# Optimization experiments

Hardware: AMD Instinct MI355X
Metric: run time of the kernel (lower is better)

Reference implementation:

```python
import jax, jax.numpy as jnp
import numpy as np

H = 64      # hidden_size
L = 4       # num_layers
IN = 28     # input_size
OUT = 10    # output classes


def setup_inputs() -> dict:
    key = jax.random.key(0)
    ks = jax.random.split(key, 2 + 4 * L + 2)
    B, T = 4096, 256
    inp = {"x": jax.random.normal(ks[0], (B, T, IN), jnp.float32)}
    s = 1.0 / np.sqrt(H).astype(np.float32)  # PyTorch LSTM init range
    k = 1
    for l in range(L):
        d_in = IN if l == 0 else H
        inp[f"W_ih{l}"] = jax.random.uniform(ks[k], (4 * H, d_in), jnp.float32, -s, s); k += 1
        inp[f"W_hh{l}"] = jax.random.uniform(ks[k], (4 * H, H), jnp.float32, -s, s); k += 1
        inp[f"b_ih{l}"] = jax.random.uniform(ks[k], (4 * H,), jnp.float32, -s, s); k += 1
        inp[f"b_hh{l}"] = jax.random.uniform(ks[k], (4 * H,), jnp.float32, -s, s); k += 1
    so = 1.0 / np.sqrt(H).astype(np.float32)
    inp["W_out"] = jax.random.uniform(ks[k], (OUT, H), jnp.float32, -so, so); k += 1
    inp["b_out"] = jax.random.uniform(ks[k], (OUT,), jnp.float32, -so, so)
    return inp


def _lstm_layer(x, W_ih, W_hh, b_ih, b_hh):
    # x: [B, T, D] -> h sequence [B, T, H]. PyTorch gate order: i, f, g, o.
    B = x.shape[0]
    gx = jnp.einsum('btd,gd->btg', x, W_ih) + (b_ih + b_hh)  # precompute input gates [B,T,4H]

    def step(carry, gxt):
        h, c = carry
        g = gxt + h @ W_hh.T                      # [B, 4H]
        i = jax.nn.sigmoid(g[:, 0*H:1*H])
        f = jax.nn.sigmoid(g[:, 1*H:2*H])
        gg = jnp.tanh(g[:, 2*H:3*H])
        o = jax.nn.sigmoid(g[:, 3*H:4*H])
        c = f * c + i * gg
        h = o * jnp.tanh(c)
        return (h, c), h

    init = (jnp.zeros((B, H), x.dtype), jnp.zeros((B, H), x.dtype))
    _, hs = jax.lax.scan(step, init, gx.swapaxes(0, 1))  # [T, B, H]
    return hs.swapaxes(0, 1)


def reference(x, W_ih0, W_hh0, b_ih0, b_hh0, W_ih1, W_hh1, b_ih1, b_hh1,
              W_ih2, W_hh2, b_ih2, b_hh2, W_ih3, W_hh3, b_ih3, b_hh3,
              W_out, b_out):
    params = [(W_ih0, W_hh0, b_ih0, b_hh0), (W_ih1, W_hh1, b_ih1, b_hh1),
              (W_ih2, W_hh2, b_ih2, b_hh2), (W_ih3, W_hh3, b_ih3, b_hh3)]
    h = x
    for (W_ih, W_hh, b_ih, b_hh) in params:
        h = _lstm_layer(h, W_ih, W_hh, b_ih, b_hh)
    # final linear on last timestep: r_out[:, -1, :] @ W_out.T + b_out
    return h[:, -1, :] @ W_out.T + b_out
```

## Files before the change

### kernel.cpp

```cpp
#include <hip/hip_runtime.h>

#define TS    256
#define ROWS  16
#define DIN   28

typedef _Float16 f16x4 __attribute__((ext_vector_type(4)));
typedef float    f32x4 __attribute__((ext_vector_type(4)));

#if __has_builtin(__builtin_amdgcn_rcpf)
#define RCPF(x) __builtin_amdgcn_rcpf(x)
#else
#define RCPF(x) (1.0f / (x))
#endif
#if __has_builtin(__builtin_amdgcn_exp2f)
#define EXP2F(x) __builtin_amdgcn_exp2f(x)
#else
#define EXP2F(x) exp2f(x)
#endif

__device__ __forceinline__ float sigm(float x) {
  return RCPF(1.0f + EXP2F(x * -1.44269504f));
}
__device__ __forceinline__ float tanhf_(float x) {
  return 1.0f - 2.0f * RCPF(1.0f + EXP2F(x * 2.885390082f));
}
__device__ __forceinline__ f16x4 cvt4(float a, float b, float c, float d) {
  f16x4 r; r[0] = (_Float16)a; r[1] = (_Float16)b; r[2] = (_Float16)c; r[3] = (_Float16)d;
  return r;
}
__device__ __forceinline__ f16x4 cvt4v(float4 v) { return cvt4(v.x, v.y, v.z, v.w); }

#define MFMA16(a, b, c) __builtin_amdgcn_mfma_f32_16x16x16f16((a), (b), (c), 0, 0, 0)

__global__ __launch_bounds__(1024, 4) void lstm4_pipe(
    const float* __restrict__ x,
    const float* __restrict__ Wih0, const float* __restrict__ Whh0,
    const float* __restrict__ bih0, const float* __restrict__ bhh0,
    const float* __restrict__ Wih1, const float* __restrict__ Whh1,
    const float* __restrict__ bih1, const float* __restrict__ bhh1,
    const float* __restrict__ Wih2, const float* __restrict__ Whh2,
    const float* __restrict__ bih2, const float* __restrict__ bhh2,
    const float* __restrict__ Wih3, const float* __restrict__ Whh3,
    const float* __restrict__ bih3, const float* __restrict__ bhh3,
    const float* __restrict__ Wout, const float* __restrict__ bout,
    float* __restrict__ out)
{
  const int tid  = (int)threadIdx.x;
  const int lane = tid & 63;
  const int w    = tid >> 6;
  const int l    = w >> 2;
  const int wv   = w & 3;
  const int r    = lane & 15;
  const int q    = lane >> 4;
  const int r0   = (int)blockIdx.x * ROWS;

  __shared__ _Float16 hbuf[4][2][ROWS][72];

  for (int i = tid; i < 4 * 2 * ROWS * 72; i += 1024)
    (&hbuf[0][0][0][0])[i] = (_Float16)0.0f;

  const float* Wih = (l == 0) ? Wih0 : (l == 1) ? Wih1 : (l == 2) ? Wih2 : Wih3;
  const float* Whh = (l == 0) ? Whh0 : (l == 1) ? Whh1 : (l == 2) ? Whh2 : Whh3;
  const float* bih = (l == 0) ? bih0 : (l == 1) ? bih1 : (l == 2) ? bih2 : bih3;
  const float* bhh = (l == 0) ? bhh0 : (l == 1) ? bhh1 : (l == 2) ? bhh2 : bhh3;

  f16x4 wx[4][4];
  f16x4 wh[4][4];
  float bv[4];

#pragma unroll
  for (int nt = 0; nt < 4; ++nt) {
    const int col = 64 * nt + 16 * wv + r;
    if (l == 0) {
      wx[nt][0] = cvt4v(*(const float4*)&Wih[col * DIN + 4 * q]);
      wx[nt][1] = (q < 3) ? cvt4v(*(const float4*)&Wih[col * DIN + 16 + 4 * q])
                          : cvt4(0.f, 0.f, 0.f, 0.f);
      wx[nt][2] = cvt4(0.f, 0.f, 0.f, 0.f);
      wx[nt][3] = cvt4(0.f, 0.f, 0.f, 0.f);
    } else {
#pragma unroll
      for (int s = 0; s < 4; ++s)
        wx[nt][s] = cvt4v(*(const float4*)&Wih[col * 64 + 16 * s + 4 * q]);
    }
#pragma unroll
    for (int s = 0; s < 4; ++s)
      wh[nt][s] = cvt4v(*(const float4*)&Whh[col * 64 + 16 * s + 4 * q]);
    bv[nt] = bih[col] + bhh[col];
  }

  const float* xrow = x + (size_t)(r0 + r) * (TS * DIN);
  f16x4 xa0 = cvt4(0.f, 0.f, 0.f, 0.f), xa1 = cvt4(0.f, 0.f, 0.f, 0.f);
  if (l == 0) {
    xa0 = cvt4v(*(const float4*)&xrow[4 * q]);
    if (q < 3) xa1 = cvt4v(*(const float4*)&xrow[16 + 4 * q]);
  }

  f32x4 cst = f32x4{0.f, 0.f, 0.f, 0.f};

  for (int s = 0; s < TS + 3; ++s) {
    __syncthreads();
    const int t = s - l;
    if (t < 0 || t >= TS) continue;
    const int pi = t & 1;

    f32x4 acc[4];
#pragma unroll
    for (int nt = 0; nt < 4; ++nt)
      acc[nt] = f32x4{bv[nt], bv[nt], bv[nt], bv[nt]};

    if (l == 0) {
#pragma unroll
      for (int nt = 0; nt < 4; ++nt) acc[nt] = MFMA16(xa0, wx[nt][0], acc[nt]);
#pragma unroll
      for (int nt = 0; nt < 4; ++nt) acc[nt] = MFMA16(xa1, wx[nt][1], acc[nt]);
      if (t + 1 < TS) {
        const float4 v0 = *(const float4*)&xrow[(t + 1) * DIN + 4 * q];
        float4 v1 = make_float4(0.f, 0.f, 0.f, 0.f);
        if (q < 3) v1 = *(const float4*)&xrow[(t + 1) * DIN + 16 + 4 * q];
        xa0 = cvt4v(v0);
        xa1 = cvt4v(v1);
      }
    } else {
      const _Float16* pin = &hbuf[l - 1][pi][r][4 * q];
#pragma unroll
      for (int s2 = 0; s2 < 4; ++s2) {
        const f16x4 a = *(const f16x4*)&pin[16 * s2];
#pragma unroll
        for (int nt = 0; nt < 4; ++nt) acc[nt] = MFMA16(a, wx[nt][s2], acc[nt]);
      }
    }
    {
      const _Float16* prc = &hbuf[l][pi ^ 1][r][4 * q];
#pragma unroll
      for (int s2 = 0; s2 < 4; ++s2) {
        const f16x4 a = *(const f16x4*)&prc[16 * s2];
#pragma unroll
        for (int nt = 0; nt < 4; ++nt) acc[nt] = MFMA16(a, wh[nt][s2], acc[nt]);
      }
    }

    _Float16* pw = &hbuf[l][pi][4 * q][16 * wv + r];
#pragma unroll
    for (int j = 0; j < 4; ++j) {
      const float ig = sigm(acc[0][j]);
      const float fg = sigm(acc[1][j]);
      const float gg = tanhf_(acc[2][j]);
      const float og = sigm(acc[3][j]);
      const float c  = fg * cst[j] + ig * gg;
      cst[j] = c;
      pw[j * 72] = (_Float16)(og * tanhf_(c));
    }
  }

  __syncthreads();

  if (tid < 160) {
    const int rr = tid & 15;
    const int oc = tid >> 4;
    float a = bout[oc];
#pragma unroll 16
    for (int k = 0; k < 64; ++k)
      a += (float)hbuf[3][1][rr][k] * Wout[oc * 64 + k];
    out[(size_t)(r0 + rr) * 10 + oc] = a;
  }
}

extern "C" void kernel_launch(void* const* d_in, const int* in_sizes, int n_in,
                              void* d_out, int out_size, void* d_ws, size_t ws_size,
                              hipStream_t stream) {
  (void)in_sizes; (void)n_in; (void)d_ws; (void)ws_size; (void)out_size;
  lstm4_pipe<<<dim3(4096 / ROWS), dim3(1024), 0, stream>>>(
      (const float*)d_in[0],
      (const float*)d_in[1],  (const float*)d_in[2],  (const float*)d_in[3],  (const float*)d_in[4],
      (const float*)d_in[5],  (const float*)d_in[6],  (const float*)d_in[7],  (const float*)d_in[8],
      (const float*)d_in[9],  (const float*)d_in[10], (const float*)d_in[11], (const float*)d_in[12],
      (const float*)d_in[13], (const float*)d_in[14], (const float*)d_in[15], (const float*)d_in[16],
      (const float*)d_in[17], (const float*)d_in[18],
      (float*)d_out);
}
```

Before: 505.6 us.

## Replace per-step block barriers with LDS flag sync and use 16x16x32 MFMA

Drops the block-wide __syncthreads per wavefront step. Each layer's waves now wait on per-wave shared-memory progress flags, written with release stores and read by spin-waits, and the h buffer grows to a 4-slot ring so layers can drift up to a few timesteps apart. It also switches to the 16x16x32 f16 MFMA, halving the number of matrix instructions, and moves the next-x global load ahead of the wait. The risks are spin-wait polling overhead and subtle memory-ordering correctness with the volatile flag reads.

```diff
diff --git a/kernel.cpp b/kernel.cpp
--- a/kernel.cpp
+++ b/kernel.cpp
@@ -4,7 +4,7 @@
 #define ROWS  16
 #define DIN   28
 
-typedef _Float16 f16x4 __attribute__((ext_vector_type(4)));
+typedef _Float16 f16x8 __attribute__((ext_vector_type(8)));
 typedef float    f32x4 __attribute__((ext_vector_type(4)));
 
 #if __has_builtin(__builtin_amdgcn_rcpf)
@@ -24,15 +24,26 @@
 __device__ __forceinline__ float tanhf_(float x) {
   return 1.0f - 2.0f * RCPF(1.0f + EXP2F(x * 2.885390082f));
 }
-__device__ __forceinline__ f16x4 cvt4(float a, float b, float c, float d) {
-  f16x4 r; r[0] = (_Float16)a; r[1] = (_Float16)b; r[2] = (_Float16)c; r[3] = (_Float16)d;
+__device__ __forceinline__ f16x8 cvt8(float4 a, float4 b) {
+  f16x8 r;
+  r[0] = (_Float16)a.x; r[1] = (_Float16)a.y; r[2] = (_Float16)a.z; r[3] = (_Float16)a.w;
+  r[4] = (_Float16)b.x; r[5] = (_Float16)b.y; r[6] = (_Float16)b.z; r[7] = (_Float16)b.w;
   return r;
 }
-__device__ __forceinline__ f16x4 cvt4v(float4 v) { return cvt4(v.x, v.y, v.z, v.w); }
-
-#define MFMA16(a, b, c) __builtin_amdgcn_mfma_f32_16x16x16f16((a), (b), (c), 0, 0, 0)
-
-__global__ __launch_bounds__(1024, 4) void lstm4_pipe(
+
+#define MFMA32(a, b, c) __builtin_amdgcn_mfma_f32_16x16x32_f16((a), (b), (c), 0, 0, 0)
+
+__device__ __forceinline__ int imin(int a, int b) { return a < b ? a : b; }
+
+__device__ __forceinline__ void wait4(volatile int* f, int T) {
+  int a = f[0], b = f[1], c = f[2], d = f[3];
+  while (imin(imin(a, b), imin(c, d)) < T) {
+    __builtin_amdgcn_s_sleep(1);
+    a = f[0]; b = f[1]; c = f[2]; d = f[3];
+  }
+}
+
+__global__ __launch_bounds__(1024, 4) void lstm4_flags(
     const float* __restrict__ x,
     const float* __restrict__ Wih0, const float* __restrict__ Whh0,
     const float* __restrict__ bih0, const float* __restrict__ bhh0,
@@ -54,92 +65,101 @@
   const int q    = lane >> 4;
   const int r0   = (int)blockIdx.x * ROWS;
 
-  __shared__ _Float16 hbuf[4][2][ROWS][72];
-
-  for (int i = tid; i < 4 * 2 * ROWS * 72; i += 1024)
+  __shared__ _Float16 hbuf[4][4][ROWS][72] __attribute__((aligned(16)));
+  __shared__ int flags[4][4][4] __attribute__((aligned(16)));
+
+  for (int i = tid; i < 4 * 4 * ROWS * 72; i += 1024)
     (&hbuf[0][0][0][0])[i] = (_Float16)0.0f;
+  if (tid < 64) (&flags[0][0][0])[tid] = -1;
+  __syncthreads();
 
   const float* Wih = (l == 0) ? Wih0 : (l == 1) ? Wih1 : (l == 2) ? Wih2 : Wih3;
   const float* Whh = (l == 0) ? Whh0 : (l == 1) ? Whh1 : (l == 2) ? Whh2 : Whh3;
   const float* bih = (l == 0) ? bih0 : (l == 1) ? bih1 : (l == 2) ? bih2 : bih3;
   const float* bhh = (l == 0) ? bhh0 : (l == 1) ? bhh1 : (l == 2) ? bhh2 : bhh3;
 
-  f16x4 wx[4][4];
-  f16x4 wh[4][4];
+  f16x8 wx[4][2];
+  f16x8 wh[4][2];
   float bv[4];
 
 #pragma unroll
   for (int nt = 0; nt < 4; ++nt) {
     const int col = 64 * nt + 16 * wv + r;
     if (l == 0) {
-      wx[nt][0] = cvt4v(*(const float4*)&Wih[col * DIN + 4 * q]);
-      wx[nt][1] = (q < 3) ? cvt4v(*(const float4*)&Wih[col * DIN + 16 + 4 * q])
-                          : cvt4(0.f, 0.f, 0.f, 0.f);
-      wx[nt][2] = cvt4(0.f, 0.f, 0.f, 0.f);
-      wx[nt][3] = cvt4(0.f, 0.f, 0.f, 0.f);
+      const float4 a = *(const float4*)&Wih[col * DIN + 8 * q];
+      float4 b = make_float4(0.f, 0.f, 0.f, 0.f);
+      if (q < 3) b = *(const float4*)&Wih[col * DIN + 8 * q + 4];
+      wx[nt][0] = cvt8(a, b);
+      wx[nt][1] = cvt8(make_float4(0, 0, 0, 0), make_float4(0, 0, 0, 0));
     } else {
 #pragma unroll
-      for (int s = 0; s < 4; ++s)
-        wx[nt][s] = cvt4v(*(const float4*)&Wih[col * 64 + 16 * s + 4 * q]);
-    }
-#pragma unroll
-    for (int s = 0; s < 4; ++s)
-      wh[nt][s] = cvt4v(*(const float4*)&Whh[col * 64 + 16 * s + 4 * q]);
+      for (int kt = 0; kt < 2; ++kt)
+        wx[nt][kt] = cvt8(*(const float4*)&Wih[col * 64 + kt * 32 + 8 * q],
+                          *(const float4*)&Wih[col * 64 + kt * 32 + 8 * q + 4]);
+    }
+#pragma unroll
+    for (int kt = 0; kt < 2; ++kt)
+      wh[nt][kt] = cvt8(*(const float4*)&Whh[col * 64 + kt * 32 + 8 * q],
+                        *(const float4*)&Whh[col * 64 + kt * 32 + 8 * q + 4]);
     bv[nt] = bih[col] + bhh[col];
   }
 
   const float* xrow = x + (size_t)(r0 + r) * (TS * DIN);
-  f16x4 xa0 = cvt4(0.f, 0.f, 0.f, 0.f), xa1 = cvt4(0.f, 0.f, 0.f, 0.f);
+  f16x8 xa = cvt8(make_float4(0, 0, 0, 0), make_float4(0, 0, 0, 0));
   if (l == 0) {
-    xa0 = cvt4v(*(const float4*)&xrow[4 * q]);
-    if (q < 3) xa1 = cvt4v(*(const float4*)&xrow[16 + 4 * q]);
+    const float4 a = *(const float4*)&xrow[8 * q];
+    float4 b = make_float4(0.f, 0.f, 0.f, 0.f);
+    if (q < 3) b = *(const float4*)&xrow[8 * q + 4];
+    xa = cvt8(a, b);
   }
 
   f32x4 cst = f32x4{0.f, 0.f, 0.f, 0.f};
 
-  for (int s = 0; s < TS + 3; ++s) {
-    __syncthreads();
-    const int t = s - l;
-    if (t < 0 || t >= TS) continue;
-    const int pi = t & 1;
+  for (int t = 0; t < TS; ++t) {
+    const int sl = t & 3, sp = (t - 1) & 3;
+
+    float4 nx0 = make_float4(0, 0, 0, 0), nx1 = make_float4(0, 0, 0, 0);
+    if (l == 0 && t + 1 < TS) {
+      nx0 = *(const float4*)&xrow[(t + 1) * DIN + 8 * q];
+      if (q < 3) nx1 = *(const float4*)&xrow[(t + 1) * DIN + 8 * q + 4];
+    }
+
+    if (l < 3) wait4(&flags[l + 1][sl][0], t - 4);
+    if (l > 0) wait4(&flags[l - 1][sl][0], t);
+    wait4(&flags[l][sp][0], t - 1);
+    __threadfence_block();
 
     f32x4 acc[4];
 #pragma unroll
     for (int nt = 0; nt < 4; ++nt)
       acc[nt] = f32x4{bv[nt], bv[nt], bv[nt], bv[nt]};
 
+    const _Float16* prc = &hbuf[l][sp][r][8 * q];
+    const f16x8 arc0 = *(const f16x8*)(prc);
+    const f16x8 arc1 = *(const f16x8*)(prc + 32);
+
     if (l == 0) {
 #pragma unroll
-      for (int nt = 0; nt < 4; ++nt) acc[nt] = MFMA16(xa0, wx[nt][0], acc[nt]);
-#pragma unroll
-      for (int nt = 0; nt < 4; ++nt) acc[nt] = MFMA16(xa1, wx[nt][1], acc[nt]);
-      if (t + 1 < TS) {
-        const float4 v0 = *(const float4*)&xrow[(t + 1) * DIN + 4 * q];
-        float4 v1 = make_float4(0.f, 0.f, 0.f, 0.f);
-        if (q < 3) v1 = *(const float4*)&xrow[(t + 1) * DIN + 16 + 4 * q];
-        xa0 = cvt4v(v0);
-        xa1 = cvt4v(v1);
+      for (int nt = 0; nt < 4; ++nt) {
+        acc[nt] = MFMA32(xa, wx[nt][0], acc[nt]);
+        acc[nt] = MFMA32(arc0, wh[nt][0], acc[nt]);
+        acc[nt] = MFMA32(arc1, wh[nt][1], acc[nt]);
       }
+      xa = cvt8(nx0, nx1);
     } else {
-      const _Float16* pin = &hbuf[l - 1][pi][r][4 * q];
-#pragma unroll
-      for (int s2 = 0; s2 < 4; ++s2) {
-        const f16x4 a = *(const f16x4*)&pin[16 * s2];
-#pragma unroll
-        for (int nt = 0; nt < 4; ++nt) acc[nt] = MFMA16(a, wx[nt][s2], acc[nt]);
+      const _Float16* pin = &hbuf[l - 1][sl][r][8 * q];
+      const f16x8 ain0 = *(const f16x8*)(pin);
+      const f16x8 ain1 = *(const f16x8*)(pin + 32);
+#pragma unroll
+      for (int nt = 0; nt < 4; ++nt) {
+        acc[nt] = MFMA32(ain0, wx[nt][0], acc[nt]);
+        acc[nt] = MFMA32(ain1, wx[nt][1], acc[nt]);
+        acc[nt] = MFMA32(arc0, wh[nt][0], acc[nt]);
+        acc[nt] = MFMA32(arc1, wh[nt][1], acc[nt]);
       }
     }
-    {
-      const _Float16* prc = &hbuf[l][pi ^ 1][r][4 * q];
-#pragma unroll
-      for (int s2 = 0; s2 < 4; ++s2) {
-        const f16x4 a = *(const f16x4*)&prc[16 * s2];
-#pragma unroll
-        for (int nt = 0; nt < 4; ++nt) acc[nt] = MFMA16(a, wh[nt][s2], acc[nt]);
-      }
-    }
-
-    _Float16* pw = &hbuf[l][pi][4 * q][16 * wv + r];
+
+    _Float16* pw = &hbuf[l][sl][4 * q][16 * wv + r];
 #pragma unroll
     for (int j = 0; j < 4; ++j) {
       const float ig = sigm(acc[0][j]);
@@ -150,6 +170,9 @@
       cst[j] = c;
       pw[j * 72] = (_Float16)(og * tanhf_(c));
     }
+
+    if (lane == 0)
+      __hip_atomic_store(&flags[l][sl][wv], t, __ATOMIC_RELEASE, __HIP_MEMORY_SCOPE_WORKGROUP);
   }
 
   __syncthreads();
@@ -160,7 +183,7 @@
     float a = bout[oc];
 #pragma unroll 16
     for (int k = 0; k < 64; ++k)
-      a += (float)hbuf[3][1][rr][k] * Wout[oc * 64 + k];
+      a += (float)hbuf[3][3][rr][k] * Wout[oc * 64 + k];
     out[(size_t)(r0 + rr) * 10 + oc] = a;
   }
 }
@@ -169,7 +192,7 @@
                               void* d_out, int out_size, void* d_ws, size_t ws_size,
                               hipStream_t stream) {
   (void)in_sizes; (void)n_in; (void)d_ws; (void)ws_size; (void)out_size;
-  lstm4_pipe<<<dim3(4096 / ROWS), dim3(1024), 0, stream>>>(
+  lstm4_flags<<<dim3(4096 / ROWS), dim3(1024), 0, stream>>>(
       (const float*)d_in[0],
       (const float*)d_in[1],  (const float*)d_in[2],  (const float*)d_in[3],  (const float*)d_in[4],
       (const float*)d_in[5],  (const float*)d_in[6],  (const float*)d_in[7],  (const float*)d_in[8],
```

Measured after the change: 512.7 us. Within noise of the previous version (+1.4%).

## Use one wave per layer with 16x16x32 f16 MFMA

Applied to the files above, without the earlier changes.

The work split changes from four waves per LSTM layer (1024 threads) to one wave per layer (256 threads). Each wave now computes all 16 gate/column tiles of its layer. Matrix math moves from 16x16x16 to 16x16x32 f16 MFMA, which halves the instruction count, and uses 8-wide LDS loads. The goal is cheaper block barriers and denser MFMA issue in the layer-diagonal pipeline. The cost is much higher register pressure (all weights held in VGPRs) and a single wave per SIMD, so latency hiding and overlap of transcendental work with MFMA issue are reduced.

```diff
diff --git a/kernel.cpp b/kernel.cpp
--- a/kernel.cpp
+++ b/kernel.cpp
@@ -4,7 +4,7 @@
 #define ROWS  16
 #define DIN   28
 
-typedef _Float16 f16x4 __attribute__((ext_vector_type(4)));
+typedef _Float16 f16x8 __attribute__((ext_vector_type(8)));
 typedef float    f32x4 __attribute__((ext_vector_type(4)));
 
 #if __has_builtin(__builtin_amdgcn_rcpf)
@@ -24,15 +24,17 @@
 __device__ __forceinline__ float tanhf_(float x) {
   return 1.0f - 2.0f * RCPF(1.0f + EXP2F(x * 2.885390082f));
 }
-__device__ __forceinline__ f16x4 cvt4(float a, float b, float c, float d) {
-  f16x4 r; r[0] = (_Float16)a; r[1] = (_Float16)b; r[2] = (_Float16)c; r[3] = (_Float16)d;
+
+__device__ __forceinline__ f16x8 cvt8(float4 a, float4 b) {
+  f16x8 r;
+  r[0] = (_Float16)a.x; r[1] = (_Float16)a.y; r[2] = (_Float16)a.z; r[3] = (_Float16)a.w;
+  r[4] = (_Float16)b.x; r[5] = (_Float16)b.y; r[6] = (_Float16)b.z; r[7] = (_Float16)b.w;
   return r;
 }
-__device__ __forceinline__ f16x4 cvt4v(float4 v) { return cvt4(v.x, v.y, v.z, v.w); }
 
-#define MFMA16(a, b, c) __builtin_amdgcn_mfma_f32_16x16x16f16((a), (b), (c), 0, 0, 0)
+#define MFMA32(a, b, c) __builtin_amdgcn_mfma_f32_16x16x32_f16((a), (b), (c), 0, 0, 0)
 
-__global__ __launch_bounds__(1024, 4) void lstm4_pipe(
+__global__ __launch_bounds__(256, 1) void lstm4_diag2(
     const float* __restrict__ x,
     const float* __restrict__ Wih0, const float* __restrict__ Whh0,
     const float* __restrict__ bih0, const float* __restrict__ bhh0,
@@ -47,108 +49,119 @@
 {
   const int tid  = (int)threadIdx.x;
   const int lane = tid & 63;
-  const int w    = tid >> 6;
-  const int l    = w >> 2;
-  const int wv   = w & 3;
+  const int l    = tid >> 6;
   const int r    = lane & 15;
   const int q    = lane >> 4;
   const int r0   = (int)blockIdx.x * ROWS;
 
-  __shared__ _Float16 hbuf[4][2][ROWS][72];
+  __shared__ _Float16 hbuf[4][2][ROWS][72] __attribute__((aligned(16)));
 
-  for (int i = tid; i < 4 * 2 * ROWS * 72; i += 1024)
+  for (int i = tid; i < 4 * 2 * ROWS * 72; i += 256)
     (&hbuf[0][0][0][0])[i] = (_Float16)0.0f;
+  __syncthreads();
 
   const float* Wih = (l == 0) ? Wih0 : (l == 1) ? Wih1 : (l == 2) ? Wih2 : Wih3;
   const float* Whh = (l == 0) ? Whh0 : (l == 1) ? Whh1 : (l == 2) ? Whh2 : Whh3;
   const float* bih = (l == 0) ? bih0 : (l == 1) ? bih1 : (l == 2) ? bih2 : bih3;
   const float* bhh = (l == 0) ? bhh0 : (l == 1) ? bhh1 : (l == 2) ? bhh2 : bhh3;
 
-  f16x4 wx[4][4];
-  f16x4 wh[4][4];
-  float bv[4];
+  f16x8 wx[4][4][2];
+  f16x8 wh[4][4][2];
+  float bv[4][4];
 
 #pragma unroll
-  for (int nt = 0; nt < 4; ++nt) {
-    const int col = 64 * nt + 16 * wv + r;
-    if (l == 0) {
-      wx[nt][0] = cvt4v(*(const float4*)&Wih[col * DIN + 4 * q]);
-      wx[nt][1] = (q < 3) ? cvt4v(*(const float4*)&Wih[col * DIN + 16 + 4 * q])
-                          : cvt4(0.f, 0.f, 0.f, 0.f);
-      wx[nt][2] = cvt4(0.f, 0.f, 0.f, 0.f);
-      wx[nt][3] = cvt4(0.f, 0.f, 0.f, 0.f);
-    } else {
+  for (int g = 0; g < 4; ++g) {
 #pragma unroll
-      for (int s = 0; s < 4; ++s)
-        wx[nt][s] = cvt4v(*(const float4*)&Wih[col * 64 + 16 * s + 4 * q]);
+    for (int ct = 0; ct < 4; ++ct) {
+      const int col = 64 * g + 16 * ct + r;
+      if (l == 0) {
+        const float* wp = &Wih[col * DIN + 8 * q];
+        const float4 a = *(const float4*)wp;
+        float4 b = make_float4(0.f, 0.f, 0.f, 0.f);
+        if (q < 3) b = *(const float4*)(wp + 4);
+        wx[g][ct][0] = cvt8(a, b);
+        f16x8 z{}; wx[g][ct][1] = z;
+      } else {
+        const float* wp = &Wih[col * 64 + 8 * q];
+        wx[g][ct][0] = cvt8(*(const float4*)wp, *(const float4*)(wp + 4));
+        wx[g][ct][1] = cvt8(*(const float4*)(wp + 32), *(const float4*)(wp + 36));
+      }
+      const float* hp = &Whh[col * 64 + 8 * q];
+      wh[g][ct][0] = cvt8(*(const float4*)hp, *(const float4*)(hp + 4));
+      wh[g][ct][1] = cvt8(*(const float4*)(hp + 32), *(const float4*)(hp + 36));
+      bv[g][ct] = bih[col] + bhh[col];
     }
-#pragma unroll
-    for (int s = 0; s < 4; ++s)
-      wh[nt][s] = cvt4v(*(const float4*)&Whh[col * 64 + 16 * s + 4 * q]);
-    bv[nt] = bih[col] + bhh[col];
   }
 
   const float* xrow = x + (size_t)(r0 + r) * (TS * DIN);
-  f16x4 xa0 = cvt4(0.f, 0.f, 0.f, 0.f), xa1 = cvt4(0.f, 0.f, 0.f, 0.f);
+  float4 nx0 = make_float4(0.f, 0.f, 0.f, 0.f), nx1 = nx0;
   if (l == 0) {
-    xa0 = cvt4v(*(const float4*)&xrow[4 * q]);
-    if (q < 3) xa1 = cvt4v(*(const float4*)&xrow[16 + 4 * q]);
+    nx0 = *(const float4*)&xrow[8 * q];
+    if (q < 3) nx1 = *(const float4*)&xrow[8 * q + 4];
   }
 
-  f32x4 cst = f32x4{0.f, 0.f, 0.f, 0.f};
+  f32x4 cst[4];
+#pragma unroll
+  for (int ct = 0; ct < 4; ++ct) cst[ct] = f32x4{0.f, 0.f, 0.f, 0.f};
 
   for (int s = 0; s < TS + 3; ++s) {
     __syncthreads();
     const int t = s - l;
     if (t < 0 || t >= TS) continue;
-    const int pi = t & 1;
+    const int sl = t & 1;
+    const int sp = sl ^ 1;
 
-    f32x4 acc[4];
-#pragma unroll
-    for (int nt = 0; nt < 4; ++nt)
-      acc[nt] = f32x4{bv[nt], bv[nt], bv[nt], bv[nt]};
-
+    f16x8 xa{};
     if (l == 0) {
-#pragma unroll
-      for (int nt = 0; nt < 4; ++nt) acc[nt] = MFMA16(xa0, wx[nt][0], acc[nt]);
-#pragma unroll
-      for (int nt = 0; nt < 4; ++nt) acc[nt] = MFMA16(xa1, wx[nt][1], acc[nt]);
+      xa = cvt8(nx0, nx1);
       if (t + 1 < TS) {
-        const float4 v0 = *(const float4*)&xrow[(t + 1) * DIN + 4 * q];
-        float4 v1 = make_float4(0.f, 0.f, 0.f, 0.f);
-        if (q < 3) v1 = *(const float4*)&xrow[(t + 1) * DIN + 16 + 4 * q];
-        xa0 = cvt4v(v0);
-        xa1 = cvt4v(v1);
-      }
-    } else {
-      const _Float16* pin = &hbuf[l - 1][pi][r][4 * q];
-#pragma unroll
-      for (int s2 = 0; s2 < 4; ++s2) {
-        const f16x4 a = *(const f16x4*)&pin[16 * s2];
-#pragma unroll
-        for (int nt = 0; nt < 4; ++nt) acc[nt] = MFMA16(a, wx[nt][s2], acc[nt]);
-      }
-    }
-    {
-      const _Float16* prc = &hbuf[l][pi ^ 1][r][4 * q];
-#pragma unroll
-      for (int s2 = 0; s2 < 4; ++s2) {
-        const f16x4 a = *(const f16x4*)&prc[16 * s2];
-#pragma unroll
-        for (int nt = 0; nt < 4; ++nt) acc[nt] = MFMA16(a, wh[nt][s2], acc[nt]);
+        const float* xp = &xrow[(t + 1) * DIN + 8 * q];
+        nx0 = *(const float4*)xp;
+        nx1 = (q < 3) ? *(const float4*)(xp + 4) : make_float4(0.f, 0.f, 0.f, 0.f);
       }
     }
 
-    _Float16* pw = &hbuf[l][pi][4 * q][16 * wv + r];
+    const _Float16* prc = &hbuf[l][sp][r][8 * q];
+    const f16x8 arc0 = *(const f16x8*)prc;
+    const f16x8 arc1 = *(const f16x8*)(prc + 32);
+    f16x8 ain0{}, ain1{};
+    if (l > 0) {
+      const _Float16* pin = &hbuf[l - 1][sl][r][8 * q];
+      ain0 = *(const f16x8*)pin;
+      ain1 = *(const f16x8*)(pin + 32);
+    }
+
+    f32x4 acc[4][4];
 #pragma unroll
-    for (int j = 0; j < 4; ++j) {
-      const float ig = sigm(acc[0][j]);
-      const float fg = sigm(acc[1][j]);
-      const float gg = tanhf_(acc[2][j]);
-      const float og = sigm(acc[3][j]);
-      const float c  = fg * cst[j] + ig * gg;
-      cst[j] = c;
-      pw[j * 72] = (_Float16)(og * tanhf_(c));
+    for (int g = 0; g < 4; ++g) {
+#pragma unroll
+      for (int ct = 0; ct < 4; ++ct) {
+        f32x4 a = f32x4{bv[g][ct], bv[g][ct], bv[g][ct], bv[g][ct]};
+        if (l == 0) {
+          a = MFMA32(xa, wx[g][ct][0], a);
+        } else {
+          a = MFMA32(ain0, wx[g][ct][0], a);
+          a = MFMA32(ain1, wx[g][ct][1], a);
+        }
+        a = MFMA32(arc0, wh[g][ct][0], a);
+        a = MFMA32(arc1, wh[g][ct][1], a);
+        acc[g][ct] = a;
+      }
+    }
+
+#pragma unroll
+    for (int ct = 0; ct < 4; ++ct) {
+      _Float16* pw = &hbuf[l][sl][4 * q][16 * ct + r];
+#pragma unroll
+      for (int j = 0; j < 4; ++j) {
+        const float ig = sigm(acc[0][ct][j]);
+        const float fg = sigm(acc[1][ct][j]);
+        const float gg = tanhf_(acc[2][ct][j]);
+        const float og = sigm(acc[3][ct][j]);
+        const float c  = fg * cst[ct][j] + ig * gg;
+        cst[ct][j] = c;
+        pw[j * 72] = (_Float16)(og * tanhf_(c));
+      }
     }
   }
 
@@ -169,7 +182,7 @@
                               void* d_out, int out_size, void* d_ws, size_t ws_size,
                               hipStream_t stream) {
   (void)in_sizes; (void)n_in; (void)d_ws; (void)ws_size; (void)out_size;
-  lstm4_pipe<<<dim3(4096 / ROWS), dim3(1024), 0, stream>>>(
+  lstm4_diag2<<<dim3(4096 / ROWS), dim3(256), 0, stream>>>(
       (const float*)d_in[0],
       (const float*)d_in[1],  (const float*)d_in[2],  (const float*)d_in[3],  (const float*)d_in[4],
       (const float*)d_in[5],  (const float*)d_in[6],  (const float*)d_in[7],  (const float*)d_in[8],
```

New measurement: 698.9 us. 1.38x slower.

## Process two timesteps per block barrier using per-layer LDS flag sync

Applied to the files above, without the earlier changes.

Restructures the layer-wavefront pipeline so each block-wide barrier advances two timesteps per layer. Within a pair, the four waves of a layer sync among themselves through shared-memory release flags and a spin-wait instead of a full __syncthreads. The h buffer grows to four slots per layer, and the x prefetch loads two timesteps ahead. This is meant to halve the number of block-wide barriers on the serial recurrence, at the cost of spin-polling overhead and more LDS.

```diff
diff --git a/kernel.cpp b/kernel.cpp
--- a/kernel.cpp
+++ b/kernel.cpp
@@ -32,7 +32,19 @@
 
 #define MFMA16(a, b, c) __builtin_amdgcn_mfma_f32_16x16x16f16((a), (b), (c), 0, 0, 0)
 
-__global__ __launch_bounds__(1024, 4) void lstm4_pipe(
+#define ST_REL(p, v) __hip_atomic_store((p), (v), __ATOMIC_RELEASE, __HIP_MEMORY_SCOPE_WORKGROUP)
+
+__device__ __forceinline__ int imin(int a, int b) { return a < b ? a : b; }
+
+__device__ __forceinline__ void wait4(volatile const int* f, int T) {
+  int a = f[0], b = f[1], c = f[2], d = f[3];
+  while (imin(imin(a, b), imin(c, d)) < T) {
+    __builtin_amdgcn_s_sleep(1);
+    a = f[0]; b = f[1]; c = f[2]; d = f[3];
+  }
+}
+
+__global__ __launch_bounds__(1024, 4) void lstm4_p2(
     const float* __restrict__ x,
     const float* __restrict__ Wih0, const float* __restrict__ Whh0,
     const float* __restrict__ bih0, const float* __restrict__ bhh0,
@@ -54,10 +66,13 @@
   const int q    = lane >> 4;
   const int r0   = (int)blockIdx.x * ROWS;
 
-  __shared__ _Float16 hbuf[4][2][ROWS][72];
-
-  for (int i = tid; i < 4 * 2 * ROWS * 72; i += 1024)
+  __shared__ _Float16 hbuf[4][4][ROWS][72] __attribute__((aligned(16)));
+  __shared__ int mflag[4][4];
+
+  for (int i = tid; i < 4 * 4 * ROWS * 72; i += 1024)
     (&hbuf[0][0][0][0])[i] = (_Float16)0.0f;
+  if (tid < 16) (&mflag[0][0])[tid] = -1;
+  __syncthreads();
 
   const float* Wih = (l == 0) ? Wih0 : (l == 1) ? Wih1 : (l == 2) ? Wih2 : Wih3;
   const float* Whh = (l == 0) ? Whh0 : (l == 1) ? Whh1 : (l == 2) ? Whh2 : Whh3;
@@ -67,7 +82,6 @@
   f16x4 wx[4][4];
   f16x4 wh[4][4];
   float bv[4];
-
 #pragma unroll
   for (int nt = 0; nt < 4; ++nt) {
     const int col = 64 * nt + 16 * wv + r;
@@ -89,66 +103,128 @@
   }
 
   const float* xrow = x + (size_t)(r0 + r) * (TS * DIN);
-  f16x4 xa0 = cvt4(0.f, 0.f, 0.f, 0.f), xa1 = cvt4(0.f, 0.f, 0.f, 0.f);
+  float4 pxa0 = make_float4(0.f, 0.f, 0.f, 0.f), pxa1 = pxa0, pxb0 = pxa0, pxb1 = pxa0;
   if (l == 0) {
-    xa0 = cvt4v(*(const float4*)&xrow[4 * q]);
-    if (q < 3) xa1 = cvt4v(*(const float4*)&xrow[16 + 4 * q]);
+    pxa0 = *(const float4*)&xrow[4 * q];
+    if (q < 3) pxa1 = *(const float4*)&xrow[16 + 4 * q];
+    pxb0 = *(const float4*)&xrow[DIN + 4 * q];
+    if (q < 3) pxb1 = *(const float4*)&xrow[DIN + 16 + 4 * q];
   }
 
   f32x4 cst = f32x4{0.f, 0.f, 0.f, 0.f};
 
-  for (int s = 0; s < TS + 3; ++s) {
+  for (int P = 0; P < TS / 2 + 3; ++P) {
     __syncthreads();
-    const int t = s - l;
-    if (t < 0 || t >= TS) continue;
-    const int pi = t & 1;
-
-    f32x4 acc[4];
-#pragma unroll
-    for (int nt = 0; nt < 4; ++nt)
-      acc[nt] = f32x4{bv[nt], bv[nt], bv[nt], bv[nt]};
-
+    const int T = 2 * (P - l);
+    if (T < 0 || T >= TS) continue;
+
+    f16x4 xaA0{}, xaA1{}, xaB0{}, xaB1{};
     if (l == 0) {
-#pragma unroll
-      for (int nt = 0; nt < 4; ++nt) acc[nt] = MFMA16(xa0, wx[nt][0], acc[nt]);
-#pragma unroll
-      for (int nt = 0; nt < 4; ++nt) acc[nt] = MFMA16(xa1, wx[nt][1], acc[nt]);
-      if (t + 1 < TS) {
-        const float4 v0 = *(const float4*)&xrow[(t + 1) * DIN + 4 * q];
-        float4 v1 = make_float4(0.f, 0.f, 0.f, 0.f);
-        if (q < 3) v1 = *(const float4*)&xrow[(t + 1) * DIN + 16 + 4 * q];
-        xa0 = cvt4v(v0);
-        xa1 = cvt4v(v1);
-      }
-    } else {
-      const _Float16* pin = &hbuf[l - 1][pi][r][4 * q];
-#pragma unroll
-      for (int s2 = 0; s2 < 4; ++s2) {
-        const f16x4 a = *(const f16x4*)&pin[16 * s2];
-#pragma unroll
-        for (int nt = 0; nt < 4; ++nt) acc[nt] = MFMA16(a, wx[nt][s2], acc[nt]);
-      }
-    }
+      xaA0 = cvt4v(pxa0); xaA1 = cvt4v(pxa1);
+      xaB0 = cvt4v(pxb0); xaB1 = cvt4v(pxb1);
+    }
+
+    const int sA = T & 3;
+    const int sR = (T - 1) & 3;
+    const int sB = (T + 1) & 3;
+
     {
-      const _Float16* prc = &hbuf[l][pi ^ 1][r][4 * q];
-#pragma unroll
-      for (int s2 = 0; s2 < 4; ++s2) {
-        const f16x4 a = *(const f16x4*)&prc[16 * s2];
-#pragma unroll
-        for (int nt = 0; nt < 4; ++nt) acc[nt] = MFMA16(a, wh[nt][s2], acc[nt]);
-      }
-    }
-
-    _Float16* pw = &hbuf[l][pi][4 * q][16 * wv + r];
-#pragma unroll
-    for (int j = 0; j < 4; ++j) {
-      const float ig = sigm(acc[0][j]);
-      const float fg = sigm(acc[1][j]);
-      const float gg = tanhf_(acc[2][j]);
-      const float og = sigm(acc[3][j]);
-      const float c  = fg * cst[j] + ig * gg;
-      cst[j] = c;
-      pw[j * 72] = (_Float16)(og * tanhf_(c));
+      f32x4 acc[4];
+#pragma unroll
+      for (int nt = 0; nt < 4; ++nt)
+        acc[nt] = f32x4{bv[nt], bv[nt], bv[nt], bv[nt]};
+
+      if (l == 0) {
+#pragma unroll
+        for (int nt = 0; nt < 4; ++nt) acc[nt] = MFMA16(xaA0, wx[nt][0], acc[nt]);
+#pragma unroll
+        for (int nt = 0; nt < 4; ++nt) acc[nt] = MFMA16(xaA1, wx[nt][1], acc[nt]);
+      } else {
+        const _Float16* pin = &hbuf[l - 1][sA][r][4 * q];
+#pragma unroll
+        for (int s2 = 0; s2 < 4; ++s2) {
+          const f16x4 a = *(const f16x4*)&pin[16 * s2];
+#pragma unroll
+          for (int nt = 0; nt < 4; ++nt) acc[nt] = MFMA16(a, wx[nt][s2], acc[nt]);
+        }
+      }
+      {
+        const _Float16* prc = &hbuf[l][sR][r][4 * q];
+#pragma unroll
+        for (int s2 = 0; s2 < 4; ++s2) {
+          const f16x4 a = *(const f16x4*)&prc[16 * s2];
+#pragma unroll
+          for (int nt = 0; nt < 4; ++nt) acc[nt] = MFMA16(a, wh[nt][s2], acc[nt]);
+        }
+      }
+
+      _Float16* pw = &hbuf[l][sA][4 * q][16 * wv + r];
+#pragma unroll
+      for (int j = 0; j < 4; ++j) {
+        const float ig = sigm(acc[0][j]);
+        const float fg = sigm(acc[1][j]);
+        const float gg = tanhf_(acc[2][j]);
+        const float og = sigm(acc[3][j]);
+        const float c  = fg * cst[j] + ig * gg;
+        cst[j] = c;
+        pw[j * 72] = (_Float16)(og * tanhf_(c));
+      }
+    }
+
+    if (l == 0 && T + 2 < TS) {
+      const float* xp = &xrow[(T + 2) * DIN];
+      pxa0 = *(const float4*)&xp[4 * q];
+      pxa1 = (q < 3) ? *(const float4*)&xp[16 + 4 * q] : make_float4(0.f, 0.f, 0.f, 0.f);
+      pxb0 = *(const float4*)&xp[DIN + 4 * q];
+      pxb1 = (q < 3) ? *(const float4*)&xp[DIN + 16 + 4 * q] : make_float4(0.f, 0.f, 0.f, 0.f);
+    }
+
+    __threadfence_block();
+    if (lane == 0) ST_REL(&mflag[l][wv], P);
+    wait4(&mflag[l][0], P);
+    __threadfence_block();
+
+    {
+      f32x4 acc[4];
+#pragma unroll
+      for (int nt = 0; nt < 4; ++nt)
+        acc[nt] = f32x4{bv[nt], bv[nt], bv[nt], bv[nt]};
+
+      if (l == 0) {
+#pragma unroll
+        for (int nt = 0; nt < 4; ++nt) acc[nt] = MFMA16(xaB0, wx[nt][0], acc[nt]);
+#pragma unroll
+        for (int nt = 0; nt < 4; ++nt) acc[nt] = MFMA16(xaB1, wx[nt][1], acc[nt]);
+      } else {
+        const _Float16* pin = &hbuf[l - 1][sB][r][4 * q];
+#pragma unroll
+        for (int s2 = 0; s2 < 4; ++s2) {
+          const f16x4 a = *(const f16x4*)&pin[16 * s2];
+#pragma unroll
+          for (int nt = 0; nt < 4; ++nt) acc[nt] = MFMA16(a, wx[nt][s2], acc[nt]);
+        }
+      }
+      {
+        const _Float16* prc = &hbuf[l][sA][r][4 * q];
+#pragma unroll
+        for (int s2 = 0; s2 < 4; ++s2) {
+          const f16x4 a = *(const f16x4*)&prc[16 * s2];
+#pragma unroll
+          for (int nt = 0; nt < 4; ++nt) acc[nt] = MFMA16(a, wh[nt][s2], acc[nt]);
+        }
+      }
+
+      _Float16* pw = &hbuf[l][sB][4 * q][16 * wv + r];
+#pragma unroll
+      for (int j = 0; j < 4; ++j) {
+        const float ig = sigm(acc[0][j]);
+        const float fg = sigm(acc[1][j]);
+        const float gg = tanhf_(acc[2][j]);
+        const float og = sigm(acc[3][j]);
+        const float c  = fg * cst[j] + ig * gg;
+        cst[j] = c;
+        pw[j * 72] = (_Float16)(og * tanhf_(c));
+      }
     }
   }
 
@@ -160,7 +236,7 @@
     float a = bout[oc];
 #pragma unroll 16
     for (int k = 0; k < 64; ++k)
-      a += (float)hbuf[3][1][rr][k] * Wout[oc * 64 + k];
+      a += (float)hbuf[3][3][rr][k] * Wout[oc * 64 + k];
     out[(size_t)(r0 + rr) * 10 + oc] = a;
   }
 }
@@ -169,7 +245,7 @@
                               void* d_out, int out_size, void* d_ws, size_t ws_size,
                               hipStream_t stream) {
   (void)in_sizes; (void)n_in; (void)d_ws; (void)ws_size; (void)out_size;
-  lstm4_pipe<<<dim3(4096 / ROWS), dim3(1024), 0, stream>>>(
+  lstm4_p2<<<dim3(4096 / ROWS), dim3(1024), 0, stream>>>(
       (const float*)d_in[0],
       (const float*)d_in[1],  (const float*)d_in[2],  (const float*)d_in[3],  (const float*)d_in[4],
       (const float*)d_in[5],  (const float*)d_in[6],  (const float*)d_in[7],  (const float*)d_in[8],
```

New measurement: 987.9 us. 95.4% more time.
